# Performance work log

Measured on AMD Instinct MI355X. Metric: run time of the kernel, lower is better.

Reference implementation:

```python
import jax, jax.numpy as jnp
import numpy as np

D_MODEL, D_STATE, D_CONV, EXPAND = 1024, 16, 4, 2
D_INNER = EXPAND * D_MODEL
BATCH, SEQ = 2, 2048


def setup_inputs() -> dict:
    key = jax.random.key(0)
    ks = jax.random.split(key, 10)
    s = lambda fan_in: 1.0 / np.sqrt(fan_in)
    return {
        "x": jax.random.normal(ks[0], (BATCH, SEQ, D_MODEL), jnp.float32),
        "W_in": jax.random.normal(ks[1], (2 * D_INNER, D_MODEL), jnp.float32) * s(D_MODEL),
        "w_conv": jax.random.normal(ks[2], (D_INNER, D_CONV), jnp.float32) * s(D_CONV),
        "b_conv": jax.random.normal(ks[3], (D_INNER,), jnp.float32) * 0.02,
        "W_x": jax.random.normal(ks[4], (D_INNER + 2 * D_STATE, D_INNER), jnp.float32) * s(D_INNER),
        "W_dt": jax.random.normal(ks[5], (D_INNER, D_INNER), jnp.float32) * s(D_INNER),
        "b_dt": jax.random.normal(ks[6], (D_INNER,), jnp.float32) * 0.02,
        "A_log": jnp.log(jax.random.uniform(ks[7], (D_INNER, D_STATE), jnp.float32, 1e-4, 1.0)),
        "D": jnp.ones((D_INNER,), jnp.float32),
        "W_out": jax.random.normal(ks[8], (D_MODEL, D_INNER), jnp.float32) * s(D_INNER),
    }


def _depthwise_causal_conv(x, w, b):
    # x: (B, L, C), w: (C, K), causal (left-pad K-1), matches conv1d(padding=K-1)[..., :L]
    K = w.shape[1]
    L = x.shape[1]
    xp = jnp.pad(x, ((0, 0), (K - 1, 0), (0, 0)))
    out = b
    for k in range(K):  # K is tiny (4)
        out = out + xp[:, k:k + L, :] * w[:, k]
    return out


def _selective_scan(x, delta, Bm, Cm, A, Dv):
    # x, delta: (B, L, d_inner); Bm, Cm: (B, L, d_state)
    def step(state, inp):
        x_t, d_t, B_t, C_t = inp  # (B,d_inner),(B,d_inner),(B,d_state),(B,d_state)
        decay = jnp.exp(d_t[..., None] * A)          # (B, d_inner, d_state)
        state = decay * state + B_t[:, None, :] * x_t[..., None]
        y_t = jnp.einsum('bds,bs->bd', state, C_t) + x_t * Dv
        return state, y_t

    init = jnp.zeros((x.shape[0], x.shape[2], A.shape[1]), x.dtype)
    xs = tuple(jnp.swapaxes(a, 0, 1) for a in (x, delta, Bm, Cm))
    _, ys = jax.lax.scan(step, init, xs)             # ys: (L, B, d_inner)
    return jnp.swapaxes(ys, 0, 1)


def reference(x, W_in, w_conv, b_conv, W_x, W_dt, b_dt, A_log, D, W_out):
    silu = jax.nn.silu
    xz = x @ W_in.T                                   # (B, L, 2*d_inner)
    x_inner, z = jnp.split(xz, 2, axis=-1)
    x_conv = silu(_depthwise_causal_conv(x_inner, w_conv, b_conv))
    x_dbl = x_conv @ W_x.T                            # (B, L, d_inner + 2*d_state)
    delta, Bm, Cm = jnp.split(x_dbl, [D_INNER, D_INNER + D_STATE], axis=-1)
    delta = jax.nn.softplus(delta @ W_dt.T + b_dt)
    A = -jnp.exp(A_log.astype(jnp.float32))
    y = _selective_scan(x_conv, delta, Bm, Cm, A, D)
    y = y * silu(z)
    return y @ W_out.T
```

## Files before the change

kernel.cpp:

```cpp
#include <hip/hip_runtime.h>
#include <hip/hip_bf16.h>


#define BATCH 2
#define SEQ   2048
#define DM    1024
#define DI    2048
#define DS    16
#define T_TOK (BATCH * SEQ)

#define CL 64
#define NC 32

typedef __bf16 v8bf __attribute__((ext_vector_type(8)));
typedef float  v4f  __attribute__((ext_vector_type(4)));

__device__ __forceinline__ void gld16(const void* g, void* l) {
    __builtin_amdgcn_global_load_lds(
        (const __attribute__((address_space(1))) void*)g,
        (__attribute__((address_space(3))) void*)l, 16, 0, 0);
}

__device__ __forceinline__ float b2f(__hip_bfloat16 v) { return __bfloat162float(v); }

__global__ void detect_dtype(const unsigned* __restrict__ Dptr, int* __restrict__ flag) {
    if (threadIdx.x == 0 && blockIdx.x == 0)
        *flag = (Dptr[0] == 0x3F803F80u) ? 1 : 0;
}

__device__ __forceinline__ float load_in(const void* p, size_t i, int isbf) {
    return isbf ? b2f(((const __hip_bfloat16*)p)[i]) : ((const float*)p)[i];
}

#define NBIG0 (T_TOK * DM)
#define NBIG1 (4096 * DM)
#define NBIG2 (DI * DI)
#define NBIG3 (DM * DI)
__global__ void convert_big(const void* __restrict__ s0, const void* __restrict__ s1,
                            const void* __restrict__ s2, const void* __restrict__ s3,
                            __hip_bfloat16* __restrict__ d0, __hip_bfloat16* __restrict__ d1,
                            __hip_bfloat16* __restrict__ d2, __hip_bfloat16* __restrict__ d3,
                            const int* __restrict__ flag) {
    if (*flag) return;
    size_t e = ((size_t)blockIdx.x * 256 + threadIdx.x) * 8;
    const float* src; __hip_bfloat16* dst;
    if (e < NBIG0)                      { src = (const float*)s0 + e;                 dst = d0 + e; }
    else if (e < NBIG0 + NBIG1)         { e -= NBIG0; src = (const float*)s1 + e;     dst = d1 + e; }
    else if (e < NBIG0 + NBIG1 + NBIG2) { e -= NBIG0 + NBIG1; src = (const float*)s2 + e; dst = d2 + e; }
    else                                { e -= NBIG0 + NBIG1 + NBIG2; src = (const float*)s3 + e; dst = d3 + e; }
    const float4 a = *(const float4*)src;
    const float4 b = *(const float4*)(src + 4);
    __bf16 o[8] = {(__bf16)a.x,(__bf16)a.y,(__bf16)a.z,(__bf16)a.w,
                   (__bf16)b.x,(__bf16)b.y,(__bf16)b.z,(__bf16)b.w};
    *(uint4*)dst = *(uint4*)&o[0];
}

__global__ void convert_small(const void* __restrict__ wconv, const void* __restrict__ bconv,
                              const void* __restrict__ bdt, const void* __restrict__ dv,
                              __hip_bfloat16* __restrict__ wconvb, __hip_bfloat16* __restrict__ bconvb,
                              __hip_bfloat16* __restrict__ bdtb, __hip_bfloat16* __restrict__ db,
                              const int* __restrict__ flag) {
    const int isbf = *flag;
    const int i = blockIdx.x * 256 + threadIdx.x;
    if (i < 8192)        wconvb[i]        = __float2bfloat16(load_in(wconv, i, isbf));
    else if (i < 10240)  bconvb[i - 8192] = __float2bfloat16(load_in(bconv, i - 8192, isbf));
    else if (i < 12288)  bdtb[i - 10240]  = __float2bfloat16(load_in(bdt, i - 10240, isbf));
    else if (i < 14336)  db[i - 12288]    = __float2bfloat16(load_in(dv, i - 12288, isbf));
}

template <int MODE, int TM, int TN>
__global__ __launch_bounds__(256) void gemm_bt(
    const __hip_bfloat16* __restrict__ Ac, const void* __restrict__ Araw,
    const __hip_bfloat16* __restrict__ Bc, const void* __restrict__ Braw,
    void* __restrict__ out0, void* __restrict__ out1,
    const __hip_bfloat16* __restrict__ bias,
    const int* __restrict__ flag,
    int M, int N, int K, int LDK)
{
    constexpr int MF = TM / 32;
    constexpr int NF = TN / 32;
    constexpr int ASLOT = TM * 4;
    constexpr int BSLOT = TN * 4;
    __shared__ v8bf Asv[2 * ASLOT];
    __shared__ v8bf Bsv[2 * BSLOT];

    const int isbf = *flag;
    const __hip_bfloat16* A  = (isbf && Araw) ? (const __hip_bfloat16*)Araw : Ac;
    const __hip_bfloat16* Bw = (isbf && Braw) ? (const __hip_bfloat16*)Braw : Bc;

    const int nx = gridDim.x;
    const int nblk = nx * gridDim.y;
    const int id = blockIdx.y * nx + blockIdx.x;
    const int sid = (id & 7) * (nblk >> 3) + (id >> 3);
    const int bxs = sid % nx;
    const int bys = sid / nx;

    const int tid  = threadIdx.x;
    const int bm   = bys * TM;
    const int bn   = bxs * TN;
    const int w    = tid >> 6;
    const int lane = tid & 63;
    const int wm   = (w >> 1) * (TM / 2);
    const int wn   = (w & 1) * (TN / 2);
    const int lrow  = lane & 15;
    const int lquad = lane >> 4;

    const int koff = (MODE == 4) ? blockIdx.z * K : 0;

    v4f acc[MF][NF];
#pragma unroll
    for (int i = 0; i < MF; i++)
#pragma unroll
        for (int j = 0; j < NF; j++) acc[i][j] = (v4f){0.f, 0.f, 0.f, 0.f};

    const int r0 = tid >> 2;
    const int q0 = (tid & 3) ^ ((r0 >> 1) & 3);
    const __hip_bfloat16* gA0 = A  + (size_t)(bm + r0) * LDK + koff + q0 * 8;
    const __hip_bfloat16* gA1 = A  + (size_t)(bm + 64 + r0) * LDK + koff + q0 * 8;
    const __hip_bfloat16* gB0 = Bw + (size_t)(bn + r0) * LDK + koff + q0 * 8;
    const __hip_bfloat16* gB1 = Bw + (size_t)(bn + 64 + r0) * LDK + koff + q0 * 8;
    char* lA0 = (char*)Asv + tid * 16;
    char* lA1 = (char*)Asv + 4096 + tid * 16;
    char* lB0 = (char*)Bsv + tid * 16;
    char* lB1 = (char*)Bsv + 4096 + tid * 16;

    const int swz = lquad ^ ((lrow >> 1) & 3);
    int sA[MF], sB[NF];
#pragma unroll
    for (int i = 0; i < MF; i++) sA[i] = (wm + i * 16 + lrow) * 4 + swz;
#pragma unroll
    for (int i = 0; i < NF; i++) sB[i] = (wn + i * 16 + lrow) * 4 + swz;

    const int NIT = K >> 5;
    gld16(gA0, lA0);
    if (TM == 128) gld16(gA1, lA1);
    gld16(gB0, lB0);
    if (TN == 128) gld16(gB1, lB1);

    int k = 32;
    for (int it = 0; it < NIT; ++it) {
        const int cb = it & 1;
        __syncthreads();
        if (it + 1 < NIT) {
            const int pa = (cb ^ 1) * (ASLOT * 16);
            const int pb = (cb ^ 1) * (BSLOT * 16);
            gld16(gA0 + k, lA0 + pa);
            if (TM == 128) gld16(gA1 + k, lA1 + pa);
            gld16(gB0 + k, lB0 + pb);
            if (TN == 128) gld16(gB1 + k, lB1 + pb);
            k += 32;
        }
        const int ca = cb * ASLOT;
        const int cbb = cb * BSLOT;
        v8bf af[MF], bfr[NF];
#pragma unroll
        for (int i = 0; i < MF; i++)
            af[i] = Asv[ca + sA[i]];
#pragma unroll
        for (int i = 0; i < NF; i++)
            bfr[i] = Bsv[cbb + sB[i]];
#pragma unroll
        for (int mi = 0; mi < MF; mi++)
#pragma unroll
            for (int ni = 0; ni < NF; ni++)
                acc[mi][ni] = __builtin_amdgcn_mfma_f32_16x16x32_bf16(
                    af[mi], bfr[ni], acc[mi][ni], 0, 0, 0);
    }

#pragma unroll
    for (int mi = 0; mi < MF; mi++) {
#pragma unroll
        for (int ni = 0; ni < NF; ni++) {
#pragma unroll
            for (int r = 0; r < 4; r++) {
                const int grow = bm + wm + mi * 16 + lquad * 4 + r;
                const int gcol = bn + wn + ni * 16 + lrow;
                const float v = acc[mi][ni][r];
                if (MODE == 0) {
                    ((__hip_bfloat16*)out0)[(size_t)grow * N + gcol] = __float2bfloat16(v);
                } else if (MODE == 1) {
                    if (gcol < 2048) {
                        ((__hip_bfloat16*)out0)[(size_t)grow * 2048 + gcol] = __float2bfloat16(v);
                    } else if (gcol < 2080) {
                        ((float*)out1)[(size_t)grow * 32 + (gcol - 2048)] = v;
                    }
                } else if (MODE == 2) {
                    const float x = v + b2f(bias[gcol]);
                    const float sp = (x > 15.f) ? x : __logf(1.f + __expf(x));
                    ((__hip_bfloat16*)out0)[(size_t)grow * 2048 + gcol] = __float2bfloat16(sp);
                } else if (MODE == 3) {
                    if (isbf)
                        ((__hip_bfloat16*)out0)[(size_t)grow * N + gcol] = __float2bfloat16(v);
                    else
                        ((float*)out0)[(size_t)grow * N + gcol] = v;
                } else {
                    ((float*)out0)[(size_t)blockIdx.z * M * N + (size_t)grow * N + gcol] = v;
                }
            }
        }
    }
}

__global__ void reduce_g4(const float* __restrict__ p, void* __restrict__ out,
                          const int* __restrict__ flag, int n) {
    const int i = (blockIdx.x * 256 + threadIdx.x) * 4;
    if (i >= n) return;
    const float4 a = *(const float4*)(p + i);
    const float4 b = *(const float4*)(p + n + i);
    const float s0 = a.x + b.x, s1 = a.y + b.y, s2 = a.z + b.z, s3 = a.w + b.w;
    if (*flag) {
        __bf16 o[4] = {(__bf16)s0, (__bf16)s1, (__bf16)s2, (__bf16)s3};
        *(uint2*)((__hip_bfloat16*)out + i) = *(uint2*)&o[0];
    } else {
        *(float4*)((float*)out + i) = make_float4(s0, s1, s2, s3);
    }
}

__global__ void prep_A(const void* __restrict__ A_log, float* __restrict__ Amat,
                       const int* __restrict__ flag) {
    const int isbf = *flag;
    const int i = blockIdx.x * 256 + threadIdx.x;
    if (i < DI * DS) Amat[i] = -__expf(load_in(A_log, i, isbf));
}

__global__ void pad_Wx(const void* __restrict__ Wx, __hip_bfloat16* __restrict__ Wxp,
                       const int* __restrict__ flag) {
    const int isbf = *flag;
    const size_t e = ((size_t)blockIdx.x * 256 + threadIdx.x) * 8;
    if (e >= (size_t)2176 * 2048) return;
    if (e >= (size_t)2080 * 2048) {
        __bf16 z[8] = {};
        *(uint4*)(Wxp + e) = *(uint4*)&z[0];
        return;
    }
    if (isbf) {
        *(uint4*)(Wxp + e) = *(const uint4*)((const __hip_bfloat16*)Wx + e);
    } else {
        const float* src = (const float*)Wx + e;
        const float4 a = *(const float4*)src;
        const float4 b = *(const float4*)(src + 4);
        __bf16 o[8] = {(__bf16)a.x,(__bf16)a.y,(__bf16)a.z,(__bf16)a.w,
                       (__bf16)b.x,(__bf16)b.y,(__bf16)b.z,(__bf16)b.w};
        *(uint4*)(Wxp + e) = *(uint4*)&o[0];
    }
}

__global__ __launch_bounds__(256) void conv_silu(
    const __hip_bfloat16* __restrict__ xz,
    const __hip_bfloat16* __restrict__ wconv,
    const __hip_bfloat16* __restrict__ bconv,
    __hip_bfloat16* __restrict__ xconv)
{
    const int idx = blockIdx.x * 256 + threadIdx.x;
    const int c8 = (idx & 255) << 3;
    const int tg = idx >> 8;
    const int tl = tg & (SEQ - 1);

    __bf16 wl[32], bl[8];
    *(uint4*)&wl[0]  = *(const uint4*)(wconv + c8 * 4);
    *(uint4*)&wl[8]  = *(const uint4*)(wconv + c8 * 4 + 8);
    *(uint4*)&wl[16] = *(const uint4*)(wconv + c8 * 4 + 16);
    *(uint4*)&wl[24] = *(const uint4*)(wconv + c8 * 4 + 24);
    *(uint4*)&bl[0]  = *(const uint4*)(bconv + c8);

    float acc[8];
#pragma unroll
    for (int cc = 0; cc < 8; cc++) acc[cc] = (float)bl[cc];

#pragma unroll
    for (int k = 0; k < 4; k++) {
        const int ts = tl - 3 + k;
        if (ts >= 0) {
            __bf16 xl[8];
            *(uint4*)&xl[0] = *(const uint4*)(xz + (size_t)(tg - 3 + k) * 4096 + c8);
#pragma unroll
            for (int cc = 0; cc < 8; cc++)
                acc[cc] += (float)wl[cc * 4 + k] * (float)xl[cc];
        }
    }

    __bf16 o[8];
#pragma unroll
    for (int cc = 0; cc < 8; cc++) {
        const float s = acc[cc] / (1.f + __expf(-acc[cc]));
        o[cc] = (__bf16)s;
    }
    *(uint4*)(xconv + (size_t)tg * DI + c8) = *(uint4*)&o[0];
}

__global__ __launch_bounds__(256) void scan_p1(
    const __hip_bfloat16* __restrict__ delta, const __hip_bfloat16* __restrict__ xconv,
    const float* __restrict__ BC, const float* __restrict__ Amat,
    float* __restrict__ Pws, float* __restrict__ Sws)
{
    const int d = blockIdx.x * 256 + threadIdx.x;
    const int c = blockIdx.y;
    const int b = blockIdx.z;
    const int tg0 = b * SEQ + c * CL;

    __shared__ float bc[CL * 32];
    for (int i = threadIdx.x; i < CL * 32; i += 256) bc[i] = BC[(size_t)tg0 * 32 + i];
    __syncthreads();

    float Areg[DS];
#pragma unroll
    for (int s = 0; s < DS; s++) Areg[s] = Amat[d * DS + s];

    float P[DS], S[DS];
#pragma unroll
    for (int s = 0; s < DS; s++) { P[s] = 1.f; S[s] = 0.f; }

    for (int i = 0; i < CL; i++) {
        const size_t tg = tg0 + i;
        const float dl = b2f(delta[tg * DI + d]);
        const float x  = b2f(xconv[tg * DI + d]);
#pragma unroll
        for (int s = 0; s < DS; s++) {
            const float e = __expf(dl * Areg[s]);
            P[s] *= e;
            S[s] = e * S[s] + bc[i * 32 + s] * x;
        }
    }

    const size_t base = (((size_t)b * NC + c) * DI + d) * DS;
#pragma unroll
    for (int s = 0; s < DS; s += 4) {
        *(float4*)(Pws + base + s) = make_float4(P[s], P[s+1], P[s+2], P[s+3]);
        *(float4*)(Sws + base + s) = make_float4(S[s], S[s+1], S[s+2], S[s+3]);
    }
}

__global__ void scan_p2(float* __restrict__ Pws, float* __restrict__ Sws) {
    const int idx = blockIdx.x * 256 + threadIdx.x;
    const int b  = idx >> 15;
    const int ds = idx & 32767;
    float carry = 0.f;
    for (int c = 0; c < NC; c++) {
        const size_t a = (((size_t)b * NC + c) << 15) + ds;
        const float p  = Pws[a];
        const float sv = Sws[a];
        Sws[a] = carry;
        carry = p * carry + sv;
    }
}

__global__ __launch_bounds__(256) void scan_p3(
    const __hip_bfloat16* __restrict__ delta, const __hip_bfloat16* __restrict__ xconv,
    const float* __restrict__ BC, const float* __restrict__ Amat,
    const float* __restrict__ Sws, const __hip_bfloat16* __restrict__ xz,
    const __hip_bfloat16* __restrict__ Dv, __hip_bfloat16* __restrict__ yg)
{
    const int d = blockIdx.x * 256 + threadIdx.x;
    const int c = blockIdx.y;
    const int b = blockIdx.z;
    const int tg0 = b * SEQ + c * CL;

    __shared__ float bc[CL * 32];
    for (int i = threadIdx.x; i < CL * 32; i += 256) bc[i] = BC[(size_t)tg0 * 32 + i];
    __syncthreads();

    float Areg[DS];
#pragma unroll
    for (int s = 0; s < DS; s++) Areg[s] = Amat[d * DS + s];

    const size_t base = (((size_t)b * NC + c) * DI + d) * DS;
    float S[DS];
#pragma unroll
    for (int s = 0; s < DS; s += 4) {
        const float4 v = *(const float4*)(Sws + base + s);
        S[s] = v.x; S[s+1] = v.y; S[s+2] = v.z; S[s+3] = v.w;
    }
    const float Dd = b2f(Dv[d]);

    for (int i = 0; i < CL; i++) {
        const size_t tg = tg0 + i;
        const float dl = b2f(delta[tg * DI + d]);
        const float x  = b2f(xconv[tg * DI + d]);
        float y = 0.f;
#pragma unroll
        for (int s = 0; s < DS; s++) {
            const float e = __expf(dl * Areg[s]);
            S[s] = e * S[s] + bc[i * 32 + s] * x;
            y += S[s] * bc[i * 32 + 16 + s];
        }
        y += x * Dd;
        const float z = b2f(xz[tg * 4096 + 2048 + d]);
        const float g = z / (1.f + __expf(-z));
        yg[tg * DI + d] = __float2bfloat16(y * g);
    }
}

extern "C" void kernel_launch(void* const* d_in, const int* in_sizes, int n_in,
                              void* d_out, int out_size, void* d_ws, size_t ws_size,
                              hipStream_t stream)
{
    const void* x_raw     = d_in[0];
    const void* W_in_raw  = d_in[1];
    const void* wconv_raw = d_in[2];
    const void* bconv_raw = d_in[3];
    const void* W_x_raw   = d_in[4];
    const void* W_dt_raw  = d_in[5];
    const void* b_dt_raw  = d_in[6];
    const void* A_log_raw = d_in[7];
    const void* D_raw     = d_in[8];
    const void* W_out_raw = d_in[9];

    char* ws = (char*)d_ws;
    size_t off = 0;
    auto alloc = [&](size_t bytes) { char* p = ws + off; off += (bytes + 255) & ~(size_t)255; return p; };
    int*            FLAG  = (int*)alloc(256);
    __hip_bfloat16* XB    = (__hip_bfloat16*)alloc((size_t)T_TOK * DM * 2);
    __hip_bfloat16* WINB  = (__hip_bfloat16*)alloc((size_t)4096 * DM * 2);
    __hip_bfloat16* WDTB  = (__hip_bfloat16*)alloc((size_t)DI * DI * 2);
    __hip_bfloat16* WOUTB = (__hip_bfloat16*)alloc((size_t)DM * DI * 2);
    __hip_bfloat16* WCONVB= (__hip_bfloat16*)alloc((size_t)DI * 4 * 2);
    __hip_bfloat16* BCONVB= (__hip_bfloat16*)alloc((size_t)DI * 2);
    __hip_bfloat16* BDTB  = (__hip_bfloat16*)alloc((size_t)DI * 2);
    __hip_bfloat16* DB    = (__hip_bfloat16*)alloc((size_t)DI * 2);
    __hip_bfloat16* XZ    = (__hip_bfloat16*)alloc((size_t)T_TOK * 4096 * 2);
    __hip_bfloat16* XCONV = (__hip_bfloat16*)alloc((size_t)T_TOK * DI * 2);
    __hip_bfloat16* DRAW  = (__hip_bfloat16*)alloc((size_t)T_TOK * DI * 2);
    __hip_bfloat16* WXPAD = (__hip_bfloat16*)alloc((size_t)2176 * DI * 2);
    float*          BC    = (float*)alloc((size_t)T_TOK * 32 * 4);
    __hip_bfloat16* DELTA = (__hip_bfloat16*)alloc((size_t)T_TOK * DI * 2);
    float*          AMAT  = (float*)alloc((size_t)DI * DS * 4);
    float*          PWS   = (float*)alloc((size_t)BATCH * NC * DI * DS * 4);
    float*          SWS   = (float*)alloc((size_t)BATCH * NC * DI * DS * 4);
    __hip_bfloat16* YG    = (__hip_bfloat16*)alloc((size_t)T_TOK * DI * 2);

    detect_dtype<<<1, 64, 0, stream>>>((const unsigned*)D_raw, FLAG);
    convert_big<<<(NBIG0 + NBIG1 + NBIG2 + NBIG3) / (256 * 8), 256, 0, stream>>>(
        x_raw, W_in_raw, W_dt_raw, W_out_raw, XB, WINB, WDTB, WOUTB, FLAG);
    convert_small<<<56, 256, 0, stream>>>(wconv_raw, bconv_raw, b_dt_raw, D_raw,
                                          WCONVB, BCONVB, BDTB, DB, FLAG);
    prep_A<<<(DI * DS + 255) / 256, 256, 0, stream>>>(A_log_raw, AMAT, FLAG);
    pad_Wx<<<(int)(((size_t)2176 * 2048 / 8 + 255) / 256), 256, 0, stream>>>(W_x_raw, WXPAD, FLAG);

    gemm_bt<0, 128, 128><<<dim3(32, 32), 256, 0, stream>>>(
        XB, x_raw, WINB, W_in_raw, XZ, nullptr, nullptr, FLAG, T_TOK, 4096, DM, DM);

    conv_silu<<<T_TOK, 256, 0, stream>>>(XZ, WCONVB, BCONVB, XCONV);

    gemm_bt<1, 64, 128><<<dim3(17, 64), 256, 0, stream>>>(
        XCONV, nullptr, WXPAD, nullptr, DRAW, BC, nullptr, FLAG, T_TOK, 2176, DI, DI);

    gemm_bt<2, 64, 128><<<dim3(16, 64), 256, 0, stream>>>(
        DRAW, nullptr, WDTB, W_dt_raw, DELTA, nullptr, BDTB, FLAG, T_TOK, DI, DI, DI);

    scan_p1<<<dim3(DI / 256, NC, BATCH), 256, 0, stream>>>(DELTA, XCONV, BC, AMAT, PWS, SWS);
    scan_p2<<<(BATCH * DI * DS) / 256, 256, 0, stream>>>(PWS, SWS);
    scan_p3<<<dim3(DI / 256, NC, BATCH), 256, 0, stream>>>(DELTA, XCONV, BC, AMAT, SWS, XZ, DB, YG);

    float* G4P = (float*)XZ;
    gemm_bt<4, 64, 128><<<dim3(8, 64, 2), 256, 0, stream>>>(
        YG, nullptr, WOUTB, W_out_raw, G4P, nullptr, nullptr, FLAG, T_TOK, DM, DI / 2, DI);
    reduce_g4<<<(T_TOK * DM / 4 + 255) / 256, 256, 0, stream>>>(G4P, d_out, FLAG, T_TOK * DM);
}
```

Baseline: 481.8 us.

## Split-K the x_proj, dt_proj and out_proj GEMMs with 128x128 tiles and reduction epilogues

```diff
diff --git a/kernel.cpp b/kernel.cpp
--- a/kernel.cpp
+++ b/kernel.cpp
@@ -55,25 +55,49 @@
     *(uint4*)dst = *(uint4*)&o[0];
 }
 
-__global__ void convert_small(const void* __restrict__ wconv, const void* __restrict__ bconv,
-                              const void* __restrict__ bdt, const void* __restrict__ dv,
-                              __hip_bfloat16* __restrict__ wconvb, __hip_bfloat16* __restrict__ bconvb,
-                              __hip_bfloat16* __restrict__ bdtb, __hip_bfloat16* __restrict__ db,
-                              const int* __restrict__ flag) {
+__global__ __launch_bounds__(256) void prep_all(
+    const void* __restrict__ Wx, __hip_bfloat16* __restrict__ Wxp,
+    const void* __restrict__ A_log, float* __restrict__ Amat,
+    const void* __restrict__ wconv, const void* __restrict__ bconv,
+    const void* __restrict__ bdt, const void* __restrict__ dv,
+    __hip_bfloat16* __restrict__ wconvb, __hip_bfloat16* __restrict__ bconvb,
+    __hip_bfloat16* __restrict__ bdtb, __hip_bfloat16* __restrict__ db,
+    const int* __restrict__ flag)
+{
     const int isbf = *flag;
-    const int i = blockIdx.x * 256 + threadIdx.x;
-    if (i < 8192)        wconvb[i]        = __float2bfloat16(load_in(wconv, i, isbf));
-    else if (i < 10240)  bconvb[i - 8192] = __float2bfloat16(load_in(bconv, i - 8192, isbf));
-    else if (i < 12288)  bdtb[i - 10240]  = __float2bfloat16(load_in(bdt, i - 10240, isbf));
-    else if (i < 14336)  db[i - 12288]    = __float2bfloat16(load_in(dv, i - 12288, isbf));
+    const int b = blockIdx.x;
+    if (b < 2176) {
+        const size_t e = ((size_t)b * 256 + threadIdx.x) * 8;
+        if (e >= (size_t)2080 * 2048) {
+            __bf16 z[8] = {};
+            *(uint4*)(Wxp + e) = *(uint4*)&z[0];
+        } else if (isbf) {
+            *(uint4*)(Wxp + e) = *(const uint4*)((const __hip_bfloat16*)Wx + e);
+        } else {
+            const float* src = (const float*)Wx + e;
+            const float4 a = *(const float4*)src;
+            const float4 c = *(const float4*)(src + 4);
+            __bf16 o[8] = {(__bf16)a.x,(__bf16)a.y,(__bf16)a.z,(__bf16)a.w,
+                           (__bf16)c.x,(__bf16)c.y,(__bf16)c.z,(__bf16)c.w};
+            *(uint4*)(Wxp + e) = *(uint4*)&o[0];
+        }
+    } else if (b < 2304) {
+        const int i = (b - 2176) * 256 + threadIdx.x;
+        Amat[i] = -__expf(load_in(A_log, i, isbf));
+    } else {
+        const int i = (b - 2304) * 256 + threadIdx.x;
+        if (i < 8192)        wconvb[i]        = __float2bfloat16(load_in(wconv, i, isbf));
+        else if (i < 10240)  bconvb[i - 8192] = __float2bfloat16(load_in(bconv, i - 8192, isbf));
+        else if (i < 12288)  bdtb[i - 10240]  = __float2bfloat16(load_in(bdt, i - 10240, isbf));
+        else if (i < 14336)  db[i - 12288]    = __float2bfloat16(load_in(dv, i - 12288, isbf));
+    }
 }
 
 template <int MODE, int TM, int TN>
 __global__ __launch_bounds__(256) void gemm_bt(
     const __hip_bfloat16* __restrict__ Ac, const void* __restrict__ Araw,
     const __hip_bfloat16* __restrict__ Bc, const void* __restrict__ Braw,
-    void* __restrict__ out0, void* __restrict__ out1,
-    const __hip_bfloat16* __restrict__ bias,
+    void* __restrict__ out0,
     const int* __restrict__ flag,
     int M, int N, int K, int LDK)
 {
@@ -178,21 +202,6 @@
                 const float v = acc[mi][ni][r];
                 if (MODE == 0) {
                     ((__hip_bfloat16*)out0)[(size_t)grow * N + gcol] = __float2bfloat16(v);
-                } else if (MODE == 1) {
-                    if (gcol < 2048) {
-                        ((__hip_bfloat16*)out0)[(size_t)grow * 2048 + gcol] = __float2bfloat16(v);
-                    } else if (gcol < 2080) {
-                        ((float*)out1)[(size_t)grow * 32 + (gcol - 2048)] = v;
-                    }
-                } else if (MODE == 2) {
-                    const float x = v + b2f(bias[gcol]);
-                    const float sp = (x > 15.f) ? x : __logf(1.f + __expf(x));
-                    ((__hip_bfloat16*)out0)[(size_t)grow * 2048 + gcol] = __float2bfloat16(sp);
-                } else if (MODE == 3) {
-                    if (isbf)
-                        ((__hip_bfloat16*)out0)[(size_t)grow * N + gcol] = __float2bfloat16(v);
-                    else
-                        ((float*)out0)[(size_t)grow * N + gcol] = v;
                 } else {
                     ((float*)out0)[(size_t)blockIdx.z * M * N + (size_t)grow * N + gcol] = v;
                 }
@@ -201,47 +210,68 @@
     }
 }
 
-__global__ void reduce_g4(const float* __restrict__ p, void* __restrict__ out,
-                          const int* __restrict__ flag, int n) {
-    const int i = (blockIdx.x * 256 + threadIdx.x) * 4;
+__global__ __launch_bounds__(256) void reduce_g2(
+    const float* __restrict__ P, __hip_bfloat16* __restrict__ draw,
+    float* __restrict__ bc)
+{
+    const int g = blockIdx.x * 256 + threadIdx.x;
+    if (g >= 4096 * 544) return;
+    const int row = g / 544;
+    const int col = (g - row * 544) * 4;
+    const size_t base = (size_t)row * 2176 + col;
+    const float4 a = *(const float4*)(P + base);
+    const float4 b = *(const float4*)(P + (size_t)4096 * 2176 + base);
+    const float s0 = a.x + b.x, s1 = a.y + b.y, s2 = a.z + b.z, s3 = a.w + b.w;
+    if (col < 2048) {
+        __bf16 o[4] = {(__bf16)s0, (__bf16)s1, (__bf16)s2, (__bf16)s3};
+        *(uint2*)(draw + (size_t)row * 2048 + col) = *(uint2*)&o[0];
+    } else if (col < 2080) {
+        *(float4*)(bc + (size_t)row * 32 + (col - 2048)) = make_float4(s0, s1, s2, s3);
+    }
+}
+
+__global__ __launch_bounds__(256) void reduce_g3(
+    const float* __restrict__ P, __hip_bfloat16* __restrict__ delta,
+    const __hip_bfloat16* __restrict__ bias)
+{
+    const size_t i = ((size_t)blockIdx.x * 256 + threadIdx.x) * 4;
+    if (i >= (size_t)4096 * 2048) return;
+    const int col = (int)(i & 2047);
+    const float4 a = *(const float4*)(P + i);
+    const float4 b = *(const float4*)(P + (size_t)4096 * 2048 + i);
+    __bf16 bb[4];
+    *(uint2*)&bb[0] = *(const uint2*)(bias + col);
+    float s[4] = {a.x + b.x + (float)bb[0], a.y + b.y + (float)bb[1],
+                  a.z + b.z + (float)bb[2], a.w + b.w + (float)bb[3]};
+    __bf16 o[4];
+#pragma unroll
+    for (int j = 0; j < 4; j++) {
+        const float x = s[j];
+        o[j] = (__bf16)((x > 15.f) ? x : __logf(1.f + __expf(x)));
+    }
+    *(uint2*)(delta + i) = *(uint2*)&o[0];
+}
+
+__global__ __launch_bounds__(256) void reduce_g4(
+    const float* __restrict__ P, void* __restrict__ out,
+    const int* __restrict__ flag)
+{
+    const size_t n = (size_t)T_TOK * DM;
+    const size_t i = ((size_t)blockIdx.x * 256 + threadIdx.x) * 4;
     if (i >= n) return;
-    const float4 a = *(const float4*)(p + i);
-    const float4 b = *(const float4*)(p + n + i);
-    const float s0 = a.x + b.x, s1 = a.y + b.y, s2 = a.z + b.z, s3 = a.w + b.w;
+    const float4 a = *(const float4*)(P + i);
+    const float4 b = *(const float4*)(P + n + i);
+    const float4 c = *(const float4*)(P + 2 * n + i);
+    const float4 d = *(const float4*)(P + 3 * n + i);
+    const float s0 = a.x + b.x + c.x + d.x;
+    const float s1 = a.y + b.y + c.y + d.y;
+    const float s2 = a.z + b.z + c.z + d.z;
+    const float s3 = a.w + b.w + c.w + d.w;
     if (*flag) {
         __bf16 o[4] = {(__bf16)s0, (__bf16)s1, (__bf16)s2, (__bf16)s3};
         *(uint2*)((__hip_bfloat16*)out + i) = *(uint2*)&o[0];
     } else {
         *(float4*)((float*)out + i) = make_float4(s0, s1, s2, s3);
-    }
-}
-
-__global__ void prep_A(const void* __restrict__ A_log, float* __restrict__ Amat,
-                       const int* __restrict__ flag) {
-    const int isbf = *flag;
-    const int i = blockIdx.x * 256 + threadIdx.x;
-    if (i < DI * DS) Amat[i] = -__expf(load_in(A_log, i, isbf));
-}
-
-__global__ void pad_Wx(const void* __restrict__ Wx, __hip_bfloat16* __restrict__ Wxp,
-                       const int* __restrict__ flag) {
-    const int isbf = *flag;
-    const size_t e = ((size_t)blockIdx.x * 256 + threadIdx.x) * 8;
-    if (e >= (size_t)2176 * 2048) return;
-    if (e >= (size_t)2080 * 2048) {
-        __bf16 z[8] = {};
-        *(uint4*)(Wxp + e) = *(uint4*)&z[0];
-        return;
-    }
-    if (isbf) {
-        *(uint4*)(Wxp + e) = *(const uint4*)((const __hip_bfloat16*)Wx + e);
-    } else {
-        const float* src = (const float*)Wx + e;
-        const float4 a = *(const float4*)src;
-        const float4 b = *(const float4*)(src + 4);
-        __bf16 o[8] = {(__bf16)a.x,(__bf16)a.y,(__bf16)a.z,(__bf16)a.w,
-                       (__bf16)b.x,(__bf16)b.y,(__bf16)b.z,(__bf16)b.w};
-        *(uint4*)(Wxp + e) = *(uint4*)&o[0];
     }
 }
 
@@ -422,37 +452,39 @@
     __hip_bfloat16* DRAW  = (__hip_bfloat16*)alloc((size_t)T_TOK * DI * 2);
     __hip_bfloat16* WXPAD = (__hip_bfloat16*)alloc((size_t)2176 * DI * 2);
     float*          BC    = (float*)alloc((size_t)T_TOK * 32 * 4);
-    __hip_bfloat16* DELTA = (__hip_bfloat16*)alloc((size_t)T_TOK * DI * 2);
     float*          AMAT  = (float*)alloc((size_t)DI * DS * 4);
     float*          PWS   = (float*)alloc((size_t)BATCH * NC * DI * DS * 4);
     float*          SWS   = (float*)alloc((size_t)BATCH * NC * DI * DS * 4);
     __hip_bfloat16* YG    = (__hip_bfloat16*)alloc((size_t)T_TOK * DI * 2);
+    float*          P23   = (float*)alloc((size_t)2 * 4096 * 2176 * 4);
+    __hip_bfloat16* DELTA = DRAW;
+    float*          G4P   = (float*)XZ;
 
     detect_dtype<<<1, 64, 0, stream>>>((const unsigned*)D_raw, FLAG);
     convert_big<<<(NBIG0 + NBIG1 + NBIG2 + NBIG3) / (256 * 8), 256, 0, stream>>>(
         x_raw, W_in_raw, W_dt_raw, W_out_raw, XB, WINB, WDTB, WOUTB, FLAG);
-    convert_small<<<56, 256, 0, stream>>>(wconv_raw, bconv_raw, b_dt_raw, D_raw,
-                                          WCONVB, BCONVB, BDTB, DB, FLAG);
-    prep_A<<<(DI * DS + 255) / 256, 256, 0, stream>>>(A_log_raw, AMAT, FLAG);
-    pad_Wx<<<(int)(((size_t)2176 * 2048 / 8 + 255) / 256), 256, 0, stream>>>(W_x_raw, WXPAD, FLAG);
+    prep_all<<<2360, 256, 0, stream>>>(W_x_raw, WXPAD, A_log_raw, AMAT,
+                                       wconv_raw, bconv_raw, b_dt_raw, D_raw,
+                                       WCONVB, BCONVB, BDTB, DB, FLAG);
 
     gemm_bt<0, 128, 128><<<dim3(32, 32), 256, 0, stream>>>(
-        XB, x_raw, WINB, W_in_raw, XZ, nullptr, nullptr, FLAG, T_TOK, 4096, DM, DM);
+        XB, x_raw, WINB, W_in_raw, XZ, FLAG, T_TOK, 4096, DM, DM);
 
     conv_silu<<<T_TOK, 256, 0, stream>>>(XZ, WCONVB, BCONVB, XCONV);
 
-    gemm_bt<1, 64, 128><<<dim3(17, 64), 256, 0, stream>>>(
-        XCONV, nullptr, WXPAD, nullptr, DRAW, BC, nullptr, FLAG, T_TOK, 2176, DI, DI);
-
-    gemm_bt<2, 64, 128><<<dim3(16, 64), 256, 0, stream>>>(
-        DRAW, nullptr, WDTB, W_dt_raw, DELTA, nullptr, BDTB, FLAG, T_TOK, DI, DI, DI);
+    gemm_bt<4, 128, 128><<<dim3(17, 32, 2), 256, 0, stream>>>(
+        XCONV, nullptr, WXPAD, nullptr, P23, FLAG, T_TOK, 2176, DI / 2, DI);
+    reduce_g2<<<(4096 * 544 + 255) / 256, 256, 0, stream>>>(P23, DRAW, BC);
+
+    gemm_bt<4, 128, 128><<<dim3(16, 32, 2), 256, 0, stream>>>(
+        DRAW, nullptr, WDTB, W_dt_raw, P23, FLAG, T_TOK, DI, DI / 2, DI);
+    reduce_g3<<<(int)(((size_t)4096 * 2048 / 4 + 255) / 256), 256, 0, stream>>>(P23, DELTA, BDTB);
 
     scan_p1<<<dim3(DI / 256, NC, BATCH), 256, 0, stream>>>(DELTA, XCONV, BC, AMAT, PWS, SWS);
     scan_p2<<<(BATCH * DI * DS) / 256, 256, 0, stream>>>(PWS, SWS);
     scan_p3<<<dim3(DI / 256, NC, BATCH), 256, 0, stream>>>(DELTA, XCONV, BC, AMAT, SWS, XZ, DB, YG);
 
-    float* G4P = (float*)XZ;
-    gemm_bt<4, 64, 128><<<dim3(8, 64, 2), 256, 0, stream>>>(
-        YG, nullptr, WOUTB, W_out_raw, G4P, nullptr, nullptr, FLAG, T_TOK, DM, DI / 2, DI);
-    reduce_g4<<<(T_TOK * DM / 4 + 255) / 256, 256, 0, stream>>>(G4P, d_out, FLAG, T_TOK * DM);
-}
+    gemm_bt<4, 128, 128><<<dim3(8, 32, 4), 256, 0, stream>>>(
+        YG, nullptr, WOUTB, W_out_raw, G4P, FLAG, T_TOK, DM, DI / 4, DI);
+    reduce_g4<<<(int)(((size_t)T_TOK * DM / 4 + 255) / 256), 256, 0, stream>>>(G4P, d_out, FLAG);
+}
```

Measured after the change: 495.6 us. 2.9% more time.
